# Performance work log

Hardware: AMD Instinct MI355X
Metric: run time of the kernel (lower is better)

Reference implementation:

```python
import jax, jax.numpy as jnp
import numpy as np

BETA = 1.0

def setup_inputs() -> dict:
    key = jax.random.key(0)
    k1, k2 = jax.random.split(key)
    N, E_DIM, N_E = 32768, 512, 8192
    z = jax.random.normal(k1, (N, E_DIM, 1, 1), dtype=jnp.float32)
    # nn.Embedding weight initialized uniform(-1, 1)
    embedding_weight = jax.random.uniform(k2, (N_E, E_DIM), dtype=jnp.float32, minval=-1.0, maxval=1.0)
    return {"z": z, "embedding_weight": embedding_weight}


def reference(z, embedding_weight):
    zf = z[:, :, 0, 0]                                  # [N, E]
    # squared euclidean distances [N, n_e]
    d = (jnp.sum(zf ** 2, axis=1, keepdims=True)
         + jnp.sum(embedding_weight ** 2, axis=1)
         - 2.0 * jnp.matmul(zf, embedding_weight.T))
    min_encoding_indices = jnp.argmin(d, axis=1)        # [N]
    z_q = embedding_weight[min_encoding_indices]        # [N, E]
    loss = (jnp.mean((jax.lax.stop_gradient(z_q) - zf) ** 2)
            + BETA * jnp.mean((z_q - jax.lax.stop_gradient(zf)) ** 2))
    # straight-through estimator
    z_q_st = zf + jax.lax.stop_gradient(z_q - zf)
    z_q_out = z_q_st[:, :, None, None]                  # [N, E, 1, 1]
    return loss, z_q_out, min_encoding_indices
```

## Files before the change

kernel.cpp:

```cpp
#include <hip/hip_runtime.h>
#include <hip/hip_fp16.h>
#include <float.h>

#define M_ROWS 32768
#define E_DIM  512
#define N_E    8192

#define BMR 64
#define NQ 4
#define EQ (N_E / NQ)

typedef __attribute__((ext_vector_type(8))) _Float16 half8;
typedef __attribute__((ext_vector_type(4))) float f32x4;

__device__ __forceinline__ void gl_lds16(const void* g, void* l) {
    __builtin_amdgcn_global_load_lds(
        (const __attribute__((address_space(1))) unsigned int*)g,
        (__attribute__((address_space(3))) unsigned int*)l, 16, 0, 0);
}

#define MFMA16(A_, B_, C_) __builtin_amdgcn_mfma_f32_16x16x32_f16((A_), (B_), (C_), 0, 0, 0)

__global__ __launch_bounds__(256) void f16_cast_kernel(const float* __restrict__ X,
                                                       ushort* __restrict__ H,
                                                       int n4) {
    int i = blockIdx.x * 256 + threadIdx.x;
    if (i >= n4) return;
    float4 v = ((const float4*)X)[i];
    float c[4] = {v.x, v.y, v.z, v.w};
    ushort hh[4];
    #pragma unroll
    for (int j = 0; j < 4; j++) {
        __half hb = __float2half(c[j]);
        hh[j] = *(ushort*)&hb;
    }
    ushort4 h = {hh[0], hh[1], hh[2], hh[3]};
    ((ushort4*)H)[i] = h;
}

__global__ __launch_bounds__(256) void pack_w_kernel(const float* __restrict__ W,
                                                     unsigned int* __restrict__ Wt) {
    __shared__ float Ws[16 * E_DIM];
    const int et = blockIdx.x;
    const int t = threadIdx.x;
    const float4* src = (const float4*)(W + (size_t)et * 16 * E_DIM);
    #pragma unroll
    for (int i = 0; i < 8; i++)
        ((float4*)Ws)[i * 256 + t] = src[i * 256 + t];
    __syncthreads();
    const int lane = t >> 2;
    const int col = lane & 15;
    const int koff = (lane >> 4) * 8 + (t & 3) * 2;
    unsigned int* dst = Wt + (size_t)et * 16 * 256 + t;
    #pragma unroll
    for (int kt = 0; kt < 16; kt++) {
        float f0 = Ws[col * E_DIM + kt * 32 + koff];
        float f1 = Ws[col * E_DIM + kt * 32 + koff + 1];
        __half h0 = __float2half(f0), h1 = __float2half(f1);
        unsigned int u = (unsigned int)(*(ushort*)&h0) | ((unsigned int)(*(ushort*)&h1) << 16);
        dst[kt * 256] = u;
    }
}

__global__ __launch_bounds__(256) void wnorm_kernel(const float* __restrict__ W,
                                                    float* __restrict__ wnorm) {
    int wave_id = (int)((blockIdx.x * blockDim.x + threadIdx.x) >> 6);
    int lane = threadIdx.x & 63;
    if (wave_id >= N_E) return;
    const float* row = W + (size_t)wave_id * E_DIM;
    float4 v0 = *(const float4*)(row + lane * 4);
    float4 v1 = *(const float4*)(row + 256 + lane * 4);
    float s = v0.x*v0.x + v0.y*v0.y + v0.z*v0.z + v0.w*v0.w
            + v1.x*v1.x + v1.y*v1.y + v1.z*v1.z + v1.w*v1.w;
    #pragma unroll
    for (int off = 32; off; off >>= 1) s += __shfl_down(s, off);
    if (lane == 0) wnorm[wave_id] = s;
}

struct Top2 { float v0, v1; int i0, i1; };

__device__ inline Top2 merge2(Top2 A, Top2 B) {
    bool af = (A.v0 < B.v0) || (A.v0 == B.v0 && A.i0 < B.i0);
    float Wv1 = af ? A.v1 : B.v1; int Wi1 = af ? A.i1 : B.i1;
    float Lv0 = af ? B.v0 : A.v0; int Li0 = af ? B.i0 : A.i0;
    bool s2 = (Wv1 < Lv0) || (Wv1 == Lv0 && Wi1 < Li0);
    Top2 R;
    R.v0 = af ? A.v0 : B.v0; R.i0 = af ? A.i0 : B.i0;
    R.v1 = s2 ? Wv1 : Lv0;   R.i1 = s2 ? Wi1 : Li0;
    return R;
}

__global__ __launch_bounds__(512, 2) void argmin_mfma(
        const ushort* __restrict__ Zh, const char* __restrict__ Wt,
        const float* __restrict__ wnorm, int* __restrict__ cand) {
    __shared__ __align__(16) char Lds[65536];

    const int t = threadIdx.x;
    const int lane = t & 63;
    const int wid = t >> 6;
    const int cg = wid & 3;
    const int rg = wid >> 2;
    const int l15 = lane & 15, l4 = lane >> 4;

    const int id = blockIdx.x;
    const int orig = (id & 7) * 256 + (id >> 3);
    const int quarter = orig >> 9;
    const int rowblk = orig & 511;
    const int row0 = rowblk * BMR;
    const int ebase = quarter * EQ;

    const int arow = (t >> 2) & 63;
    const int aswz = (t & 3) ^ ((arow >> 1) & 3);
    const ushort* Ag = Zh + (size_t)(row0 + arow) * E_DIM + ((t >> 8) & 1) * 32 + aswz * 8;
    #pragma unroll
    for (int j = 0; j < 8; j++)
        gl_lds16(Ag + j * 64, Lds + j * 8192 + t * 16);

    asm volatile("s_waitcnt vmcnt(0)" ::: "memory");
    __builtin_amdgcn_s_barrier();
    __builtin_amdgcn_sched_barrier(0);

    const int kchunk_b = (l4 ^ ((l15 >> 1) & 3)) * 16;
    half8 Areg[32];
    #pragma unroll
    for (int ks = 0; ks < 16; ks++)
        #pragma unroll
        for (int mi = 0; mi < 2; mi++)
            Areg[ks * 2 + mi] = *(const half8*)(Lds + ks * 4096
                                + (rg * 32 + mi * 16 + l15) * 64 + kchunk_b);
    asm volatile("s_waitcnt lgkmcnt(0)" ::: "memory");
    __builtin_amdgcn_sched_barrier(0);

    const char* Bp = Wt + ((size_t)(ebase >> 4) + cg) * 16384 + lane * 16;
    const float* wn_ptr = wnorm + ebase + cg * 16 + l15;

    float v0[8], v1[8];
    int i0[8], i1[8];
    #pragma unroll
    for (int q = 0; q < 8; q++) { v0[q] = FLT_MAX; v1[q] = FLT_MAX; i0[q] = 0; i1[q] = 0; }

    f32x4 acc[2];
    acc[0] = (f32x4){0.f, 0.f, 0.f, 0.f};
    acc[1] = (f32x4){0.f, 0.f, 0.f, 0.f};

    half8 Bbuf[8][2];

    #pragma unroll
    for (int p = 0; p < 7; p++) {
        Bbuf[p][0] = *(const half8*)(Bp + p * 2048);
        Bbuf[p][1] = *(const half8*)(Bp + p * 2048 + 1024);
    }

    for (int s = 0; s < 32; ++s) {
        float wn = wn_ptr[0];

        #pragma unroll
        for (int Q = 0; Q < 8; Q++) {
            __builtin_amdgcn_s_setprio(1);
            acc[0] = MFMA16(Areg[4 * Q + 0], Bbuf[Q & 7][0], acc[0]);
            acc[1] = MFMA16(Areg[4 * Q + 1], Bbuf[Q & 7][0], acc[1]);
            acc[0] = MFMA16(Areg[4 * Q + 2], Bbuf[Q & 7][1], acc[0]);
            acc[1] = MFMA16(Areg[4 * Q + 3], Bbuf[Q & 7][1], acc[1]);
            __builtin_amdgcn_s_setprio(0);
            if (s < 31 || Q < 1) {
                const char* src = Bp + ((Q + 7) >> 3) * 65536 + ((Q + 7) & 7) * 2048;
                Bbuf[(Q + 7) & 7][0] = *(const half8*)(src);
                Bbuf[(Q + 7) & 7][1] = *(const half8*)(src + 1024);
            }
        }

        {
            int col = ebase + (s * 4 + cg) * 16 + l15;
            #pragma unroll
            for (int mi = 0; mi < 2; mi++)
                #pragma unroll
                for (int r = 0; r < 4; r++) {
                    float sc = fmaf(-2.0f, acc[mi][r], wn);
                    int q = mi * 4 + r;
                    if (sc < v0[q])      { v1[q] = v0[q]; i1[q] = i0[q]; v0[q] = sc; i0[q] = col; }
                    else if (sc < v1[q]) { v1[q] = sc; i1[q] = col; }
                }
            acc[0] = (f32x4){0.f, 0.f, 0.f, 0.f};
            acc[1] = (f32x4){0.f, 0.f, 0.f, 0.f};
        }

        wn_ptr += 64;
        Bp += 65536;
    }

    __syncthreads();
    float4* SmTop = (float4*)Lds;

    #pragma unroll
    for (int mi = 0; mi < 2; mi++)
        #pragma unroll
        for (int r = 0; r < 4; r++) {
            int q = mi * 4 + r;
            Top2 T = {v0[q], v1[q], i0[q], i1[q]};
            #pragma unroll
            for (int mk = 1; mk <= 8; mk <<= 1) {
                Top2 O;
                O.v0 = __shfl_xor(T.v0, mk); O.v1 = __shfl_xor(T.v1, mk);
                O.i0 = __shfl_xor(T.i0, mk); O.i1 = __shfl_xor(T.i1, mk);
                T = merge2(T, O);
            }
            if (l15 == 0) {
                int rl = rg * 32 + mi * 16 + l4 * 4 + r;
                SmTop[rl * 4 + cg] = make_float4(T.v0, __int_as_float(T.i0), T.v1, __int_as_float(T.i1));
            }
        }
    __syncthreads();
    if (t < BMR) {
        Top2 q[4];
        #pragma unroll
        for (int j = 0; j < 4; j++) {
            float4 F = SmTop[t * 4 + j];
            q[j].v0 = F.x; q[j].i0 = __float_as_int(F.y);
            q[j].v1 = F.z; q[j].i1 = __float_as_int(F.w);
        }
        Top2 T = merge2(merge2(q[0], q[1]), merge2(q[2], q[3]));
        cand[(size_t)(row0 + t) * (2 * NQ) + quarter * 2 + 0] = T.i0;
        cand[(size_t)(row0 + t) * (2 * NQ) + quarter * 2 + 1] = T.i1;
    }
}

__global__ __launch_bounds__(256) void rescore_gather_loss(
        const float* __restrict__ Z, const float* __restrict__ W,
        const float* __restrict__ wnorm, const int* __restrict__ cand,
        float* __restrict__ out, float* __restrict__ partials) {
    const int n = blockIdx.x;
    const int t = threadIdx.x;
    const int lane = t & 63, wv = t >> 6;
    int c[8];
    #pragma unroll
    for (int j = 0; j < 8; j++) c[j] = cand[(size_t)n * 8 + j];
    float2 zv = ((const float2*)(Z + (size_t)n * E_DIM))[t];
    float2 wvv[8];
    #pragma unroll
    for (int j = 0; j < 8; j++)
        wvv[j] = ((const float2*)(W + (size_t)c[j] * E_DIM))[t];
    __shared__ float red[4][8];
    #pragma unroll
    for (int j = 0; j < 8; j++) {
        float s = zv.x * wvv[j].x + zv.y * wvv[j].y;
        #pragma unroll
        for (int off = 32; off; off >>= 1) s += __shfl_down(s, off);
        if (lane == 0) red[wv][j] = s;
    }
    __syncthreads();
    float best = FLT_MAX; int bj = 0, bc = 0x7fffffff;
    #pragma unroll
    for (int j = 0; j < 8; j++) {
        float d = red[0][j] + red[1][j] + red[2][j] + red[3][j];
        float s = wnorm[c[j]] - 2.0f * d;
        if (s < best || (s == best && c[j] < bc)) { best = s; bj = j; bc = c[j]; }
    }
    float2 wq = wvv[0];
    #pragma unroll
    for (int j = 1; j < 8; j++) if (bj == j) wq = wvv[j];
    ((float2*)(out + 1 + (size_t)n * E_DIM))[t] = wq;
    float d0 = wq.x - zv.x, d1 = wq.y - zv.y;
    float sl = d0 * d0 + d1 * d1;
    #pragma unroll
    for (int off = 32; off; off >>= 1) sl += __shfl_down(sl, off);
    __shared__ float red2[4];
    if (lane == 0) red2[wv] = sl;
    __syncthreads();
    if (t == 0) {
        partials[n] = red2[0] + red2[1] + red2[2] + red2[3];
        out[1 + (size_t)M_ROWS * E_DIM + n] = (float)bc;
    }
}

__global__ __launch_bounds__(256) void loss_reduce_kernel(const float* __restrict__ partials,
                                                          float* __restrict__ out) {
    const int t = threadIdx.x;
    float s = 0.0f;
    for (int i = t; i < M_ROWS; i += 256) s += partials[i];
    #pragma unroll
    for (int off = 32; off; off >>= 1) s += __shfl_down(s, off);
    __shared__ float red[4];
    if ((t & 63) == 0) red[t >> 6] = s;
    __syncthreads();
    if (t == 0) {
        float total = red[0] + red[1] + red[2] + red[3];
        out[0] = 2.0f * total / ((float)M_ROWS * (float)E_DIM);
    }
}

extern "C" void kernel_launch(void* const* d_in, const int* in_sizes, int n_in,
                              void* d_out, int out_size, void* d_ws, size_t ws_size,
                              hipStream_t stream) {
    const float* Z = (const float*)d_in[0];
    const float* W = (const float*)d_in[1];
    float* out = (float*)d_out;

    char* p = (char*)d_ws;
    ushort* Zh = (ushort*)p;             p += (size_t)M_ROWS * E_DIM * 2;
    unsigned int* Wt = (unsigned int*)p; p += (size_t)N_E * E_DIM * 2;
    float* wnorm = (float*)p;            p += (size_t)N_E * 4;
    int* cand = (int*)p;                 p += (size_t)M_ROWS * 8 * 4;
    float* partials = (float*)p;         p += (size_t)M_ROWS * 4;

    f16_cast_kernel<<<(M_ROWS * E_DIM / 4 + 255) / 256, 256, 0, stream>>>(Z, Zh, M_ROWS * E_DIM / 4);
    pack_w_kernel<<<N_E / 16, 256, 0, stream>>>(W, Wt);
    wnorm_kernel<<<N_E / 4, 256, 0, stream>>>(W, wnorm);
    argmin_mfma<<<NQ * (M_ROWS / BMR), 512, 0, stream>>>(Zh, (const char*)Wt, wnorm, cand);
    rescore_gather_loss<<<M_ROWS, 256, 0, stream>>>(Z, W, wnorm, cand, out, partials);
    loss_reduce_kernel<<<1, 256, 0, stream>>>(partials, out);
}
```

Measured before the change: 541.9 us.

## Stage codebook tiles through LDS with triple-buffered async global-to-LDS loads

Replaces the per-wave direct global loads of codebook fragments into registers with a cooperative triple-buffered LDS pipeline. Both row-group waves share each staged B tile, so each wave only loads a quarter of it via global_load_lds. MFMAs read their B operands from LDS, with barriers and vmcnt waits between phases. This halves redundant global/L2 traffic for B and frees registers, but adds a block barrier per half-step and raises LDS use to 96KB, which may reduce occupancy.

```diff
diff --git a/kernel.cpp b/kernel.cpp
--- a/kernel.cpp
+++ b/kernel.cpp
@@ -93,7 +93,7 @@
 __global__ __launch_bounds__(512, 2) void argmin_mfma(
         const ushort* __restrict__ Zh, const char* __restrict__ Wt,
         const float* __restrict__ wnorm, int* __restrict__ cand) {
-    __shared__ __align__(16) char Lds[65536];
+    __shared__ __align__(16) char Lds[98304];
 
     const int t = threadIdx.x;
     const int lane = t & 63;
@@ -130,9 +130,15 @@
                                 + (rg * 32 + mi * 16 + l15) * 64 + kchunk_b);
     asm volatile("s_waitcnt lgkmcnt(0)" ::: "memory");
     __builtin_amdgcn_sched_barrier(0);
-
-    const char* Bp = Wt + ((size_t)(ebase >> 4) + cg) * 16384 + lane * 16;
-    const float* wn_ptr = wnorm + ebase + cg * 16 + l15;
+    __builtin_amdgcn_s_barrier();
+    __builtin_amdgcn_sched_barrier(0);
+
+    const char* BpS = Wt + ((size_t)(ebase >> 4) + cg) * 16384 + rg * 4096 + lane * 16;
+    const char* const ldsRd = Lds + cg * 8192 + lane * 16;
+
+    int colb = ebase + cg * 16 + l15;
+    const float* wnp = wnorm + colb;
+    float wn_cur = 0.0f;
 
     float v0[8], v1[8];
     int i0[8], i1[8];
@@ -143,50 +149,68 @@
     acc[0] = (f32x4){0.f, 0.f, 0.f, 0.f};
     acc[1] = (f32x4){0.f, 0.f, 0.f, 0.f};
 
-    half8 Bbuf[8][2];
-
-    #pragma unroll
-    for (int p = 0; p < 7; p++) {
-        Bbuf[p][0] = *(const half8*)(Bp + p * 2048);
-        Bbuf[p][1] = *(const half8*)(Bp + p * 2048 + 1024);
-    }
-
-    for (int s = 0; s < 32; ++s) {
-        float wn = wn_ptr[0];
-
-        #pragma unroll
-        for (int Q = 0; Q < 8; Q++) {
-            __builtin_amdgcn_s_setprio(1);
-            acc[0] = MFMA16(Areg[4 * Q + 0], Bbuf[Q & 7][0], acc[0]);
-            acc[1] = MFMA16(Areg[4 * Q + 1], Bbuf[Q & 7][0], acc[1]);
-            acc[0] = MFMA16(Areg[4 * Q + 2], Bbuf[Q & 7][1], acc[0]);
-            acc[1] = MFMA16(Areg[4 * Q + 3], Bbuf[Q & 7][1], acc[1]);
-            __builtin_amdgcn_s_setprio(0);
-            if (s < 31 || Q < 1) {
-                const char* src = Bp + ((Q + 7) >> 3) * 65536 + ((Q + 7) & 7) * 2048;
-                Bbuf[(Q + 7) & 7][0] = *(const half8*)(src);
-                Bbuf[(Q + 7) & 7][1] = *(const half8*)(src + 1024);
-            }
-        }
-
-        {
-            int col = ebase + (s * 4 + cg) * 16 + l15;
-            #pragma unroll
-            for (int mi = 0; mi < 2; mi++)
-                #pragma unroll
-                for (int r = 0; r < 4; r++) {
-                    float sc = fmaf(-2.0f, acc[mi][r], wn);
-                    int q = mi * 4 + r;
-                    if (sc < v0[q])      { v1[q] = v0[q]; i1[q] = i0[q]; v0[q] = sc; i0[q] = col; }
-                    else if (sc < v1[q]) { v1[q] = sc; i1[q] = col; }
-                }
-            acc[0] = (f32x4){0.f, 0.f, 0.f, 0.f};
-            acc[1] = (f32x4){0.f, 0.f, 0.f, 0.f};
-        }
-
-        wn_ptr += 64;
-        Bp += 65536;
-    }
+    #define STG(SSLOT, SSREL, SH) do {                                           \
+        const char* _s = BpS + (SSREL) * 65536 + (SH) * 8192;                    \
+        char* _d = Lds + (SSLOT) * 32768 + cg * 8192 + rg * 4096;                \
+        gl_lds16(_s,        _d);                                                 \
+        gl_lds16(_s + 1024, _d + 1024);                                          \
+        gl_lds16(_s + 2048, _d + 2048);                                          \
+        gl_lds16(_s + 3072, _d + 3072);                                          \
+    } while (0)
+
+    #define PHASE(RSLOT, H, VMSTR, DOSTG, SSLOT, SSREL, SH, DOWNLD, DOFOLD) do { \
+        asm volatile("s_waitcnt " VMSTR ::: "memory");                           \
+        __builtin_amdgcn_s_barrier();                                            \
+        __builtin_amdgcn_sched_barrier(0);                                       \
+        if (DOSTG) STG(SSLOT, SSREL, SH);                                        \
+        if (DOWNLD) wn_cur = wnp[0];                                             \
+        {                                                                        \
+            const char* _b = ldsRd + (RSLOT) * 32768;                            \
+            half8 _f[8];                                                         \
+            _Pragma("unroll")                                                    \
+            for (int f = 0; f < 8; f++) _f[f] = *(const half8*)(_b + f * 1024);  \
+            __builtin_amdgcn_s_setprio(1);                                       \
+            _Pragma("unroll")                                                    \
+            for (int f = 0; f < 8; f++) {                                        \
+                acc[0] = MFMA16(Areg[((H) * 8 + f) * 2 + 0], _f[f], acc[0]);     \
+                acc[1] = MFMA16(Areg[((H) * 8 + f) * 2 + 1], _f[f], acc[1]);     \
+            }                                                                    \
+            __builtin_amdgcn_s_setprio(0);                                       \
+        }                                                                        \
+        if (DOFOLD) {                                                            \
+            _Pragma("unroll")                                                    \
+            for (int mi = 0; mi < 2; mi++)                                       \
+                _Pragma("unroll")                                                \
+                for (int r = 0; r < 4; r++) {                                    \
+                    float sc = fmaf(-2.0f, acc[mi][r], wn_cur);                  \
+                    int q = mi * 4 + r;                                          \
+                    if (sc < v0[q])      { v1[q] = v0[q]; i1[q] = i0[q]; v0[q] = sc; i0[q] = colb; } \
+                    else if (sc < v1[q]) { v1[q] = sc; i1[q] = colb; }           \
+                }                                                                \
+            acc[0] = (f32x4){0.f, 0.f, 0.f, 0.f};                                \
+            acc[1] = (f32x4){0.f, 0.f, 0.f, 0.f};                                \
+            colb += 64; wnp += 64;                                               \
+        }                                                                        \
+    } while (0)
+
+    STG(0, 0, 0);
+    STG(1, 0, 1);
+
+    for (int k = 0; k < 10; ++k) {
+        PHASE(0, 0, "vmcnt(4)", 1, 2, 1, 0, 1, 0);
+        PHASE(1, 1, "vmcnt(4)", 1, 0, 1, 1, 0, 1);
+        PHASE(2, 0, "vmcnt(4)", 1, 1, 2, 0, 1, 0);
+        PHASE(0, 1, "vmcnt(4)", 1, 2, 2, 1, 0, 1);
+        PHASE(1, 0, "vmcnt(4)", 1, 0, 3, 0, 1, 0);
+        PHASE(2, 1, "vmcnt(4)", 1, 1, 3, 1, 0, 1);
+        BpS += 3 * 65536;
+    }
+    PHASE(0, 0, "vmcnt(4)", 1, 2, 1, 0, 1, 0);
+    PHASE(1, 1, "vmcnt(4)", 1, 0, 1, 1, 0, 1);
+    PHASE(2, 0, "vmcnt(4)", 0, 0, 0, 0, 1, 0);
+    PHASE(0, 1, "vmcnt(0)", 0, 0, 0, 0, 0, 1);
+    #undef PHASE
+    #undef STG
 
     __syncthreads();
     float4* SmTop = (float4*)Lds;
```

After: 556.2 us. +2.6%, slower.
